# Performance work log

Hardware: AMD Instinct MI355X
Metric: run time of the kernel (lower is better)

## Reference

```python
import jax, jax.numpy as jnp
import numpy as np
from jax import lax

DN = ('NCHW', 'OIHW', 'NCHW')

def conv3x3(x, w, b):
    y = lax.conv_general_dilated(x, w, (1, 1), 'SAME', dimension_numbers=DN)
    return y + b[None, :, None, None]

def box_filter(x, ws):
    # depthwise WxW averaging conv, VALID after reflect pad
    C = x.shape[1]
    k = jnp.ones((C, 1, ws, ws), x.dtype) / (ws * ws)
    return lax.conv_general_dilated(x, k, (1, 1), 'VALID', feature_group_count=C,
                                    dimension_numbers=DN)

def compute_std_map(features, ws):
    N, C, H, W = features.shape
    pad = ws // 2
    fp = jnp.pad(features, ((0, 0), (0, 0), (pad, pad), (pad, pad)), mode='reflect')
    local_mean = box_filter(fp, ws)            # [N,C,H,W]
    local_mean_sq = box_filter(fp * fp, ws)
    local_var = jnp.clip(local_mean_sq - local_mean ** 2, 1e-6, None)
    if C == 4:
        cw = jax.nn.softmax(jnp.array([1.0, 1.5, 1.0, 1.5], features.dtype))
    else:
        cw = jax.nn.softmax(jnp.ones((C,), features.dtype))
    result = jnp.sum(jnp.sqrt(local_var) * cw[None, :, None, None], axis=1, keepdims=True)
    return result ** 0.8                        # [N,1,H,W]

def setup_inputs() -> dict:
    key = jax.random.key(0)
    ks = jax.random.split(key, 10)
    inp = {}
    inp['x'] = jax.random.normal(ks[0], (1, 4, 1024, 1024), jnp.float32)
    inp['w1'] = jax.random.normal(ks[1], (32, 4, 3, 3), jnp.float32) * (1.0 / np.sqrt(4 * 9))
    inp['b1'] = jax.random.normal(ks[2], (32,), jnp.float32) * 0.01
    inp['w2'] = jax.random.normal(ks[3], (16, 32, 3, 3), jnp.float32) * (1.0 / np.sqrt(32 * 9))
    inp['b2'] = jax.random.normal(ks[4], (16,), jnp.float32) * 0.01
    inp['w3'] = jax.random.normal(ks[5], (8, 16, 3, 3), jnp.float32) * (1.0 / np.sqrt(16 * 9))
    inp['b3'] = jax.random.normal(ks[6], (8,), jnp.float32) * 0.01
    inp['channel_weights'] = jnp.ones((4,), jnp.float32) / 4.0
    inp['fusion_w'] = jnp.full((1, 3, 1, 1), 1.0 / 3.0, jnp.float32) + \
        jax.random.normal(ks[7], (1, 3, 1, 1), jnp.float32) * 0.02
    inp['fusion_b'] = jnp.zeros((1,), jnp.float32)
    return inp

def reference(x, w1, b1, w2, b2, w3, b3, channel_weights, fusion_w, fusion_b):
    window_sizes = [11, 25, 49]
    # feature extractor
    f = jax.nn.leaky_relu(conv3x3(x, w1, b1), 0.2)
    f = jax.nn.leaky_relu(conv3x3(f, w2, b2), 0.2)
    f = conv3x3(f, w3, b3)                      # [B,8,H,W]
    # multi-scale std maps
    maps = jnp.concatenate([compute_std_map(f, ws) for ws in window_sizes], axis=1)  # [B,3,H,W]
    fused = jax.nn.relu(
        lax.conv_general_dilated(maps, fusion_w, (1, 1), 'VALID', dimension_numbers=DN)
        + fusion_b[None, :, None, None])        # [B,1,H,W]
    # adaptive thresholds
    std_flat = fused.reshape(-1)
    q25 = jnp.quantile(std_flat, 0.25)
    q75 = jnp.quantile(std_flat, 0.75)
    iqr75 = q75 - q25
    global_std = jnp.std(x, axis=(2, 3), keepdims=True, ddof=1)   # [B,4,1,1]
    lower = (q25 - 0.5 * iqr75) * jnp.ones_like(global_std)
    upper = (q75 + 0.5 * iqr75) * jnp.ones_like(global_std)
    gf = jnp.clip(global_std * 5.0, 0.5, 2.0)
    lower = lower * gf
    upper = upper * gf
    cwn = jax.nn.softmax(channel_weights).reshape(1, 4, 1, 1)
    channel_std = jnp.std(x * cwn, axis=(2, 3), keepdims=True, ddof=1)
    cf = jnp.clip(channel_std * 2.0, 0.8, 1.2)
    lower = lower * cf
    upper = upper * cf
    # texture mask
    q30 = jnp.quantile(std_flat, 0.3)
    q70 = jnp.quantile(std_flat, 0.7)
    lower_mean = jnp.mean(lower, axis=1, keepdims=True)           # [B,1,1,1]
    upper_mean = jnp.mean(upper, axis=1, keepdims=True)
    l_t = 0.5 * lower_mean + 0.5 * q30
    u_t = 0.5 * upper_mean + 0.5 * q70
    iqr = q70 - q30
    widen = iqr < 0.01
    l_t = jnp.where(widen, l_t - iqr, l_t)
    u_t = jnp.where(widen, u_t + iqr, u_t)
    diff = u_t - l_t
    mid0 = (l_t + u_t) / 2
    narrow = diff < 0.02
    l_t = jnp.where(narrow, mid0 - 0.01, l_t)
    u_t = jnp.where(narrow, mid0 + 0.01, u_t)
    midpoint = (l_t + u_t) / 2
    scale = u_t - l_t
    normalized = jax.nn.sigmoid(4.0 * (fused - midpoint) / scale)
    nm = jnp.mean(normalized)
    mask = jnp.where(nm > 0.65, 0.1 + 0.5 * normalized,
                     jnp.where(nm < 0.35, 0.2 + 0.5 * normalized,
                               0.15 + 0.55 * normalized))
    return mask
```

## Files before the change

### kernel.cpp

```cpp
#include <hip/hip_runtime.h>
#include <stdint.h>

constexpr int H = 1024, W = 1024;
constexpr int NPIX = H * W;
constexpr int PADM = 24;
constexpr int PROW = W + 2 * PADM;

constexpr size_t OFF_F1H   = 0;
constexpr size_t OFF_F1L   = 67108864;
constexpr size_t OFF_F2H   = 134217728;
constexpr size_t OFF_F2L   = 167772160;
constexpr size_t OFF_F3    = 0;
constexpr size_t OFF_HF    = 33554432;
constexpr size_t OFF_HF2   = 67108864;
constexpr size_t OFF_FUSED = 100663296;
constexpr size_t OFF_SMALL  = 201326592;
constexpr size_t OFF_PSTAT  = OFF_SMALL;
constexpr size_t OFF_NMSUM  = OFF_SMALL + 4096;
constexpr size_t OFF_HIST   = OFF_SMALL + 4160;
constexpr size_t OFF_RSTATE = OFF_HIST + 8192;
constexpr size_t OFF_SCAL   = OFF_RSTATE + 64;
constexpr size_t OFF_WT     = OFF_SCAL + 64;

using short8  = __attribute__((ext_vector_type(8))) short;
using short4v = __attribute__((ext_vector_type(4))) short;
using f32x4   = __attribute__((ext_vector_type(4))) float;

__device__ __forceinline__ int reflect1024(int j) {
    return j < 0 ? -j : (j > 1023 ? 2046 - j : j);
}
__device__ __forceinline__ unsigned short rne_bf16(float v) {
    uint32_t u = __float_as_uint(v);
    return (unsigned short)((u + 0x7FFFu + ((u >> 16) & 1u)) >> 16);
}
__device__ __forceinline__ float bf16f(unsigned short h) {
    return __uint_as_float(((uint32_t)h) << 16);
}

__device__ void wfrag_body(const float* __restrict__ w, unsigned short* __restrict__ wfH,
                           unsigned short* __restrict__ wfL, int CIN, int COUT, int NF, int S,
                           int blk) {
    int total = NF * S * 512;
    int e = blk * 256 + threadIdx.x;
    if (e >= total) return;
    int j = e & 7, l = (e >> 3) & 63;
    int rest = e >> 9;
    int s = rest % S, nf = rest / S;
    int k = s * 32 + ((l >> 4) << 3) + j;
    int n = (l & 15) + 16 * nf;
    float v = 0.f;
    if (k < 9 * CIN && n < COUT) {
        int kk = k / CIN, c = k % CIN;
        int ky = kk / 3, kx = kk - ky * 3;
        v = w[((n * CIN + c) * 3 + ky) * 3 + kx];
    }
    unsigned short h = rne_bf16(v);
    wfH[e] = h;
    wfL[e] = rne_bf16(v - bf16f(h));
}

__global__ void prep_kernel(const float* __restrict__ w1, const float* __restrict__ w2,
                            const float* __restrict__ w3,
                            unsigned short* wf1H, unsigned short* wf1L,
                            unsigned short* wf2H, unsigned short* wf2L,
                            unsigned short* wf3H, unsigned short* wf3L,
                            const float* __restrict__ x, double* __restrict__ pstats,
                            double* nmsum, uint32_t* hist, uint32_t* rstate) {
    __shared__ double sb1[256], sb2[256];
    const int b = blockIdx.x, tid = threadIdx.x;
    if (b == 0) {
        for (int i = tid; i < 2048; i += 256) hist[i] = 0u;
        if (tid == 0) nmsum[0] = 0.0;
        if (tid < 8) rstate[tid] = 0u;
        if (tid < 8) {
            const uint32_t ranks[8] = {262143u, 262144u, 314572u, 314573u,
                                       734002u, 734003u, 786431u, 786432u};
            rstate[8 + tid] = ranks[tid];
        }
    } else if (b < 9) {
        wfrag_body(w1, wf1H, wf1L, 4, 32, 2, 2, b - 1);
    } else if (b < 27) {
        wfrag_body(w2, wf2H, wf2L, 32, 16, 1, 9, b - 9);
    } else if (b < 37) {
        wfrag_body(w3, wf3H, wf3L, 16, 8, 1, 5, b - 27);
    } else {
        int sb = b - 37;
        int ch = sb >> 6, blk = sb & 63;
        const float* p = x + (size_t)ch * NPIX;
        double s1 = 0.0, s2 = 0.0;
        for (int i = blk * 256 + tid; i < NPIX; i += 64 * 256) {
            double v = (double)p[i];
            s1 += v; s2 += v * v;
        }
        sb1[tid] = s1; sb2[tid] = s2;
        __syncthreads();
        for (int off = 128; off > 0; off >>= 1) {
            if (tid < off) { sb1[tid] += sb1[tid + off]; sb2[tid] += sb2[tid + off]; }
            __syncthreads();
        }
        if (tid == 0) { pstats[sb * 2] = sb1[0]; pstats[sb * 2 + 1] = sb2[0]; }
    }
}

template <int CIN, int COUT, int S, bool LEAKY, int OUT_MODE, int IN_MODE, int MINW>
__global__ __launch_bounds__(256, MINW) void mconv_kernel(
        const void* __restrict__ inA, const void* __restrict__ inB,
        const unsigned short* __restrict__ wfH, const unsigned short* __restrict__ wfL,
        const float* __restrict__ bias, void* __restrict__ outA, void* __restrict__ outB) {
    constexpr int NF = (COUT + 15) / 16;
    constexpr int RS = 66 * CIN;
    __shared__ __align__(16) unsigned short Ah[6 * RS];
    __shared__ __align__(16) unsigned short Al[6 * RS];

    const int tid = threadIdx.x;
    const int bx = blockIdx.x * 64, by = blockIdx.y * 4;
    const int lane = tid & 63, rw = tid >> 6;

    if constexpr (IN_MODE == 1) {
        constexpr int CROW = RS / 8;
        constexpr int LCP  = (CIN == 32) ? 2 : 1;
        constexpr int TOT  = 12 * CROW;
        constexpr int NLOAD = (TOT + 255) / 256;
        const unsigned short* gh = (const unsigned short*)inA;
        const unsigned short* gl = (const unsigned short*)inB;

        short8 regs[NLOAD];
#pragma unroll
        for (int k = 0; k < NLOAD; ++k) {
            int idx = tid + k * 256;
            short8 v = short8{0, 0, 0, 0, 0, 0, 0, 0};
            if (idx < TOT) {
                int ar = idx / CROW;
                int j  = idx - ar * CROW;
                int r  = ar >> 1;
                int a  = ar & 1;
                int gy = by - 1 + r;
                int gx = bx - 1 + (j >> LCP);
                if ((unsigned)gy < 1024u && (unsigned)gx < 1024u) {
                    const unsigned short* g = (a ? gl : gh) +
                        ((size_t)gy << 10) * CIN + (size_t)(bx - 1) * CIN + (size_t)j * 8;
                    v = *(const short8*)g;
                }
            }
            regs[k] = v;
        }
#pragma unroll
        for (int k = 0; k < NLOAD; ++k) {
            int idx = tid + k * 256;
            if (idx < TOT) {
                int ar = idx / CROW;
                int j  = idx - ar * CROW;
                int r  = ar >> 1;
                int a  = ar & 1;
                unsigned short* dst = (a ? Al : Ah) + r * RS + j * 8;
                *(short8*)dst = regs[k];
            }
        }
    } else {
        constexpr int TOT = 6 * 4 * 66;
        constexpr int NLOAD = (TOT + 255) / 256;
        const float* xin = (const float*)inA;
        float regs[NLOAD];
#pragma unroll
        for (int k = 0; k < NLOAD; ++k) {
            int idx = tid + k * 256;
            float v = 0.f;
            if (idx < TOT) {
                int rc  = idx / 66;
                int px  = idx - rc * 66;
                int r   = rc >> 2, c = rc & 3;
                int gy = by - 1 + r, gx = bx - 1 + px;
                if ((unsigned)gy < 1024u && (unsigned)gx < 1024u)
                    v = xin[(size_t)c * NPIX + ((size_t)gy << 10) + gx];
            }
            regs[k] = v;
        }
#pragma unroll
        for (int k = 0; k < NLOAD; ++k) {
            int idx = tid + k * 256;
            if (idx < TOT) {
                int rc  = idx / 66;
                int px  = idx - rc * 66;
                int r   = rc >> 2, c = rc & 3;
                uint32_t u = __float_as_uint(regs[k]);
                Ah[r * RS + px * CIN + c] = (unsigned short)(u >> 16);
                Al[r * RS + px * CIN + c] =
                    rne_bf16(regs[k] - __uint_as_float(u & 0xFFFF0000u));
            }
        }
    }

    short8 wh[NF][S], wl[NF][S];
#pragma unroll
    for (int nf = 0; nf < NF; ++nf)
#pragma unroll
        for (int s = 0; s < S; ++s) {
            wh[nf][s] = *(const short8*)(wfH + (size_t)((nf * S + s) * 64 + lane) * 8);
            wl[nf][s] = *(const short8*)(wfL + (size_t)((nf * S + s) * 64 + lane) * 8);
        }

    const int nidx = lane & 15;
    f32x4 acc[4][NF];
#pragma unroll
    for (int nf = 0; nf < NF; ++nf) {
        float bv = (nidx + nf * 16 < COUT) ? bias[nidx + nf * 16] : 0.f;
#pragma unroll
        for (int t = 0; t < 4; ++t) acc[t][nf] = f32x4{bv, bv, bv, bv};
    }

    __syncthreads();

    if constexpr (CIN == 32) {
        const int base = rw * RS + (lane & 15) * 32 + (lane >> 4) * 8;
        const unsigned short* pah = Ah + base;
        const unsigned short* pal = Al + base;
#pragma unroll
        for (int s = 0; s < S; ++s) {
            const int ky = s / 3, kx = s - (s / 3) * 3;
#pragma unroll
            for (int t = 0; t < 4; ++t) {
                const int off = ky * RS + kx * 32 + t * 512;
                short8 a = *(const short8*)(pah + off);
                short8 b = *(const short8*)(pal + off);
#pragma unroll
                for (int nf = 0; nf < NF; ++nf) {
                    acc[t][nf] = __builtin_amdgcn_mfma_f32_16x16x32_bf16(a, wh[nf][s], acc[t][nf], 0, 0, 0);
                    acc[t][nf] = __builtin_amdgcn_mfma_f32_16x16x32_bf16(b, wh[nf][s], acc[t][nf], 0, 0, 0);
                    acc[t][nf] = __builtin_amdgcn_mfma_f32_16x16x32_bf16(a, wl[nf][s], acc[t][nf], 0, 0, 0);
                }
            }
        }
    } else if constexpr (CIN == 16) {
        const int g23 = lane >> 5;
        const int base = rw * RS + (lane & 15) * 16 + ((lane >> 4) & 1) * 8;
#pragma unroll
        for (int s = 0; s < S; ++s) {
            const int kk0 = 2 * s, kk1 = 2 * s + 1;
            const int O0 = (kk0 / 3) * RS + (kk0 - (kk0 / 3) * 3) * 16;
            const int O1 = (kk1 <= 8) ? (kk1 / 3) * RS + (kk1 - (kk1 / 3) * 3) * 16 : 0;
            const int offs = base + (g23 ? O1 : O0);
#pragma unroll
            for (int t = 0; t < 4; ++t) {
                short8 a = *(const short8*)(Ah + offs + t * 256);
                short8 b = *(const short8*)(Al + offs + t * 256);
#pragma unroll
                for (int nf = 0; nf < NF; ++nf) {
                    acc[t][nf] = __builtin_amdgcn_mfma_f32_16x16x32_bf16(a, wh[nf][s], acc[t][nf], 0, 0, 0);
                    acc[t][nf] = __builtin_amdgcn_mfma_f32_16x16x32_bf16(b, wh[nf][s], acc[t][nf], 0, 0, 0);
                    acc[t][nf] = __builtin_amdgcn_mfma_f32_16x16x32_bf16(a, wl[nf][s], acc[t][nf], 0, 0, 0);
                }
            }
        }
    } else {
        const int base = rw * RS + (lane & 15) * 4;
        const int g2 = (lane >> 4) * 2;
#pragma unroll
        for (int s = 0; s < S; ++s) {
            int kkA = s * 8 + g2, kkB = kkA + 1;
            int kyA = (kkA * 11) >> 5; int kxA = kkA - kyA * 3;
            int poA = (kkA <= 8) ? kyA * RS + kxA * 4 : 0;
            int kyB = (kkB * 11) >> 5; int kxB = kkB - kyB * 3;
            int poB = (kkB <= 8) ? kyB * RS + kxB * 4 : 0;
#pragma unroll
            for (int t = 0; t < 4; ++t) {
                union { short4v q[2]; short8 o; } ua, ub;
                ua.q[0] = *(const short4v*)(Ah + base + poA + t * 64);
                ua.q[1] = *(const short4v*)(Ah + base + poB + t * 64);
                ub.q[0] = *(const short4v*)(Al + base + poA + t * 64);
                ub.q[1] = *(const short4v*)(Al + base + poB + t * 64);
                short8 a = ua.o, b = ub.o;
#pragma unroll
                for (int nf = 0; nf < NF; ++nf) {
                    acc[t][nf] = __builtin_amdgcn_mfma_f32_16x16x32_bf16(a, wh[nf][s], acc[t][nf], 0, 0, 0);
                    acc[t][nf] = __builtin_amdgcn_mfma_f32_16x16x32_bf16(b, wh[nf][s], acc[t][nf], 0, 0, 0);
                    acc[t][nf] = __builtin_amdgcn_mfma_f32_16x16x32_bf16(a, wl[nf][s], acc[t][nf], 0, 0, 0);
                }
            }
        }
    }

    const int y = by + rw;
    const int mrow = (lane >> 4) * 4;
    if constexpr (OUT_MODE == 0) {
        __syncthreads();
        float* smem = (float*)Ah;
        if (nidx < COUT) {
#pragma unroll
            for (int t = 0; t < 4; ++t)
#pragma unroll
                for (int j = 0; j < 4; ++j) {
                    float v = acc[t][0][j];
                    if (LEAKY) v = v >= 0.f ? v : 0.2f * v;
                    smem[(nidx * 4 + rw) * 66 + t * 16 + mrow + j] = v;
                }
        }
        __syncthreads();
        float* outp = (float*)outA;
#pragma unroll
        for (int k = 0; k < COUT; ++k) {
            int i = tid + k * 256;
            int px = i & 63, r = (i >> 6) & 3, c = i >> 8;
            outp[(size_t)c * NPIX + ((size_t)(by + r) << 10) + bx + px] =
                smem[(c * 4 + r) * 66 + px];
        }
    } else {
        unsigned short* oh = (unsigned short*)outA;
        unsigned short* ol = (unsigned short*)outB;
#pragma unroll
        for (int t = 0; t < 4; ++t)
#pragma unroll
            for (int nf = 0; nf < NF; ++nf)
#pragma unroll
                for (int j = 0; j < 4; ++j) {
                    float v = acc[t][nf][j];
                    if (LEAKY) v = v >= 0.f ? v : 0.2f * v;
                    int x = bx + t * 16 + mrow + j;
                    size_t off = ((size_t)((y << 10) + x)) * COUT + nf * 16 + nidx;
                    uint32_t u = __float_as_uint(v);
                    oh[off] = (unsigned short)(u >> 16);
                    ol[off] = rne_bf16(v - __uint_as_float(u & 0xFFFF0000u));
                }
    }
}

__global__ void hbox_kernel(const float* __restrict__ f3, float* __restrict__ hf,
                            float* __restrict__ hf2, int p) {
    const int row = blockIdx.x, ch = blockIdx.y, tid = threadIdx.x;
    const float* src = f3 + ch * NPIX + row * W;
    __shared__ float sraw[PROW];
    __shared__ float Pf[PROW + 1], Pf2[PROW + 1];
    __shared__ float wtot[4], wtot2[4];

    for (int i = tid; i < PROW; i += 256)
        sraw[i] = src[reflect1024(i - PADM)];
    __syncthreads();

    float lf[5], lf2[5];
    float sf = 0.f, sf2 = 0.f;
    const int base = tid * 5;
#pragma unroll
    for (int j = 0; j < 5; ++j) {
        int idx = base + j;
        float v = (idx < PROW) ? sraw[idx] : 0.f;
        sf += v;      lf[j] = sf;
        sf2 += v * v; lf2[j] = sf2;
    }
    const int lane = tid & 63, wid = tid >> 6;
    float tf = sf, tf2 = sf2;
#pragma unroll
    for (int off = 1; off < 64; off <<= 1) {
        float a = __shfl_up(tf, off);
        float b = __shfl_up(tf2, off);
        if (lane >= off) { tf += a; tf2 += b; }
    }
    if (lane == 63) { wtot[wid] = tf; wtot2[wid] = tf2; }
    __syncthreads();
    float bse = 0.f, bse2 = 0.f;
    for (int w2 = 0; w2 < wid; ++w2) { bse += wtot[w2]; bse2 += wtot2[w2]; }
    float ex = bse + tf - sf, ex2 = bse2 + tf2 - sf2;
    if (base <= PROW) { Pf[base] = ex; Pf2[base] = ex2; }
#pragma unroll
    for (int j = 0; j < 5; ++j) {
        int idx = base + j + 1;
        if (idx <= PROW) { Pf[idx] = ex + lf[j]; Pf2[idx] = ex2 + lf2[j]; }
    }
    __syncthreads();

    float* df  = hf  + ch * NPIX + row * W;
    float* df2 = hf2 + ch * NPIX + row * W;
    for (int x = tid; x < W; x += 256) {
        int a = x + PADM - p, b = x + PADM + p + 1;
        df[x]  = Pf[b]  - Pf[a];
        df2[x] = Pf2[b] - Pf2[a];
    }
}

constexpr int VRS = 32;
__global__ __launch_bounds__(512) void vbox_kernel(const float* __restrict__ hf,
                                                   const float* __restrict__ hf2,
                                                   float* __restrict__ fused,
                                                   const float* __restrict__ fw,
                                                   const float* __restrict__ fb,
                                                   int kidx, int p, float inv_area) {
    const int tid = threadIdx.x;
    const int colIdx = tid & 63, ch = tid >> 6;
    const int col = blockIdx.x * 64 + colIdx;
    const int r0 = blockIdx.y * VRS;
    const float* pf  = hf  + ch * NPIX + col;
    const float* pf2 = hf2 + ch * NPIX + col;

    float S1 = 0.f, S2 = 0.f;
    for (int t = -p; t <= p; ++t) {
        int rr = reflect1024(r0 + t);
        S1 += pf[rr * W];
        S2 += pf2[rr * W];
    }

    const float w = fw[kidx];
    const float bias0 = fb[0];

    __shared__ float ssq[8][8][65];
    const int jj = tid >> 6, cc = tid & 63;
    for (int rb = r0; rb < r0 + VRS; rb += 8) {
#pragma unroll
        for (int j = 0; j < 8; ++j) {
            int r = rb + j;
            float m1 = S1 * inv_area, m2 = S2 * inv_area;
            float var = fmaxf(m2 - m1 * m1, 1e-6f);
            ssq[ch][j][colIdx] = sqrtf(var);
            int radd = reflect1024(r + 1 + p), rsub = reflect1024(r - p);
            S1 += pf[radd * W] - pf[rsub * W];
            S2 += pf2[radd * W] - pf2[rsub * W];
        }
        __syncthreads();
        float a = 0.f;
#pragma unroll
        for (int c8 = 0; c8 < 8; ++c8) a += ssq[c8][jj][cc];
        float m = powf(a * 0.125f, 0.8f);
        float* fp = fused + ((size_t)(rb + jj) << 10) + blockIdx.x * 64 + cc;
        if (kidx == 0)      *fp = bias0 + w * m;
        else if (kidx == 1) *fp = *fp + w * m;
        else                *fp = fmaxf(*fp + w * m, 0.f);
        __syncthreads();
    }
}

__global__ void radix_hist_kernel(const float* __restrict__ fused, uint32_t* __restrict__ hist,
                                  const uint32_t* __restrict__ rstate, int pass) {
    __shared__ uint32_t h[8][256];
    int tid = threadIdx.x;
    for (int i = tid; i < 2048; i += 256) ((uint32_t*)h)[i] = 0u;
    __syncthreads();

    uint32_t pref[8];
#pragma unroll
    for (int r = 0; r < 8; ++r) pref[r] = rstate[r];
    uint32_t maskHi = (pass == 0) ? 0u : (0xFFFFFFFFu << (32 - 8 * pass));
    int shift = 24 - 8 * pass;

    for (int i = blockIdx.x * blockDim.x + tid; i < NPIX; i += gridDim.x * blockDim.x) {
        uint32_t u = __float_as_uint(fused[i]);
        uint32_t key = (u & 0x80000000u) ? ~u : (u | 0x80000000u);
        uint32_t bin = (key >> shift) & 0xFFu;
        if (pass == 0) {
            atomicAdd(&h[0][bin], 1u);
        } else {
#pragma unroll
            for (int r = 0; r < 8; ++r) {
                if (((key ^ pref[r]) & maskHi) == 0u)
                    atomicAdd(&h[r][bin], 1u);
            }
        }
    }
    __syncthreads();
    if (pass == 0) {
        for (int i = tid; i < 256; i += 256) {
            uint32_t v = h[0][i];
            if (v)
                for (int r = 0; r < 8; ++r) atomicAdd(&hist[r * 256 + i], v);
        }
    } else {
        for (int i = tid; i < 2048; i += 256) {
            uint32_t v = ((uint32_t*)h)[i];
            if (v) atomicAdd(&hist[i], v);
        }
    }
}

__device__ __forceinline__ float key_to_float(uint32_t k) {
    uint32_t u = (k & 0x80000000u) ? (k & 0x7FFFFFFFu) : ~k;
    return __uint_as_float(u);
}

__global__ void radix_scan_kernel(uint32_t* __restrict__ hist, uint32_t* __restrict__ rstate,
                                  int pass, const double* __restrict__ pstats,
                                  const float* __restrict__ cw, float* __restrict__ scal) {
    int tid = threadIdx.x;
    int shift = 24 - 8 * pass;
    const int lane = tid & 63, wv = tid >> 6;
    __shared__ uint32_t wsum[4];
    __shared__ uint32_t fkey[8];
    for (int r = 0; r < 8; ++r) {
        uint32_t c = hist[r * 256 + tid];
        uint32_t sc = c;
#pragma unroll
        for (int off = 1; off < 64; off <<= 1) {
            uint32_t t = __shfl_up(sc, off);
            if (lane >= off) sc += t;
        }
        if (lane == 63) wsum[wv] = sc;
        __syncthreads();
        uint32_t base = 0;
        for (int w2 = 0; w2 < wv; ++w2) base += wsum[w2];
        uint32_t incl = base + sc, excl = incl - c;
        uint32_t lr = rstate[8 + r];
        if (lr >= excl && lr < incl) {
            uint32_t nk = rstate[r] | (((uint32_t)tid) << shift);
            rstate[r] = nk;
            rstate[8 + r] = lr - excl;
            if (pass == 3) fkey[r] = nk;
        }
        hist[r * 256 + tid] = 0u;
        __syncthreads();
    }

    if (pass == 3) {
        double s1 = pstats[2 * tid], s2 = pstats[2 * tid + 1];
#pragma unroll
        for (int off = 32; off > 0; off >>= 1) {
            s1 += __shfl_down(s1, off);
            s2 += __shfl_down(s2, off);
        }
        __shared__ double gs[4][2];
        if ((tid & 63) == 0) { gs[tid >> 6][0] = s1; gs[tid >> 6][1] = s2; }
        __syncthreads();
        if (tid == 0) {
            float v[8];
#pragma unroll
            for (int r = 0; r < 8; ++r) v[r] = key_to_float(fkey[r]);
            float q25 = v[0] + 0.75f * (v[1] - v[0]);
            float q30 = v[2] + 0.5f * (v[3] - v[2]);
            float q70 = v[4] + 0.5f * (v[5] - v[4]);
            float q75 = v[6] + 0.25f * (v[7] - v[6]);

            const double N = (double)NPIX;
            float gstd[4];
#pragma unroll
            for (int c = 0; c < 4; ++c) {
                double a1 = gs[c][0], a2 = gs[c][1];
                double var = (a2 - a1 * a1 / N) / (N - 1.0);
                gstd[c] = (float)sqrt(var > 0.0 ? var : 0.0);
            }
            float m = fmaxf(fmaxf(cw[0], cw[1]), fmaxf(cw[2], cw[3]));
            float e0 = expf(cw[0] - m), e1 = expf(cw[1] - m);
            float e2 = expf(cw[2] - m), e3 = expf(cw[3] - m);
            float se = e0 + e1 + e2 + e3;
            float cwn[4] = {e0 / se, e1 / se, e2 / se, e3 / se};

            float iqr75 = q75 - q25;
            float low0 = q25 - 0.5f * iqr75;
            float up0  = q75 + 0.5f * iqr75;
            float lsum = 0.f, usum = 0.f;
#pragma unroll
            for (int c = 0; c < 4; ++c) {
                float gf = fminf(fmaxf(gstd[c] * 5.f, 0.5f), 2.f);
                float cs = cwn[c] * gstd[c];
                float cf = fminf(fmaxf(cs * 2.f, 0.8f), 1.2f);
                lsum += low0 * gf * cf;
                usum += up0 * gf * cf;
            }
            float lmean = 0.25f * lsum, umean = 0.25f * usum;
            float l_t = 0.5f * lmean + 0.5f * q30;
            float u_t = 0.5f * umean + 0.5f * q70;
            float iqr = q70 - q30;
            if (iqr < 0.01f) { l_t -= iqr; u_t += iqr; }
            float diff = u_t - l_t;
            float mid0 = 0.5f * (l_t + u_t);
            if (diff < 0.02f) { l_t = mid0 - 0.01f; u_t = mid0 + 0.01f; }
            scal[0] = 0.5f * (l_t + u_t);
            scal[1] = u_t - l_t;
        }
    }
}

__global__ void sigmoid_kernel(const float* __restrict__ fused, const float* __restrict__ scal,
                               double* __restrict__ nmsum) {
    float mid = scal[0], sc = scal[1];
    float inv = 4.0f / sc;
    float local = 0.f;
    for (int i = blockIdx.x * blockDim.x + threadIdx.x; i < NPIX; i += gridDim.x * blockDim.x) {
        float t = (fused[i] - mid) * inv;
        local += 1.0f / (1.0f + expf(-t));
    }
    __shared__ float red[256];
    red[threadIdx.x] = local;
    __syncthreads();
    for (int off = 128; off > 0; off >>= 1) {
        if (threadIdx.x < off) red[threadIdx.x] += red[threadIdx.x + off];
        __syncthreads();
    }
    if (threadIdx.x == 0) atomicAdd(nmsum, (double)red[0]);
}

__global__ void final_kernel(const float* __restrict__ fused, const float* __restrict__ scal,
                             const double* __restrict__ nmsum, float* __restrict__ out) {
    float nm = (float)(nmsum[0] / (double)NPIX);
    float a, b;
    if (nm > 0.65f)      { a = 0.10f; b = 0.50f; }
    else if (nm < 0.35f) { a = 0.20f; b = 0.50f; }
    else                 { a = 0.15f; b = 0.55f; }
    float mid = scal[0], inv = 4.0f / scal[1];
    for (int i = blockIdx.x * blockDim.x + threadIdx.x; i < NPIX; i += gridDim.x * blockDim.x) {
        float t = (fused[i] - mid) * inv;
        float n = 1.0f / (1.0f + expf(-t));
        out[i] = a + b * n;
    }
}

extern "C" void kernel_launch(void* const* d_in, const int* in_sizes, int n_in,
                              void* d_out, int out_size, void* d_ws, size_t ws_size,
                              hipStream_t stream) {
    const float* x   = (const float*)d_in[0];
    const float* w1  = (const float*)d_in[1];
    const float* b1  = (const float*)d_in[2];
    const float* w2  = (const float*)d_in[3];
    const float* b2  = (const float*)d_in[4];
    const float* w3  = (const float*)d_in[5];
    const float* b3  = (const float*)d_in[6];
    const float* cw  = (const float*)d_in[7];
    const float* fw  = (const float*)d_in[8];
    const float* fb  = (const float*)d_in[9];

    char* ws = (char*)d_ws;
    unsigned short* f1h = (unsigned short*)(ws + OFF_F1H);
    unsigned short* f1l = (unsigned short*)(ws + OFF_F1L);
    unsigned short* f2h = (unsigned short*)(ws + OFF_F2H);
    unsigned short* f2l = (unsigned short*)(ws + OFF_F2L);
    float* f3    = (float*)(ws + OFF_F3);
    float* hf    = (float*)(ws + OFF_HF);
    float* hf2   = (float*)(ws + OFF_HF2);
    float* fused = (float*)(ws + OFF_FUSED);
    double* pstats = (double*)(ws + OFF_PSTAT);
    double* nmsum  = (double*)(ws + OFF_NMSUM);
    uint32_t* hist   = (uint32_t*)(ws + OFF_HIST);
    uint32_t* rstate = (uint32_t*)(ws + OFF_RSTATE);
    float* scal = (float*)(ws + OFF_SCAL);
    unsigned short* wf1H = (unsigned short*)(ws + OFF_WT);
    unsigned short* wf1L = wf1H + 2048;
    unsigned short* wf2H = wf1L + 2048;
    unsigned short* wf2L = wf2H + 4608;
    unsigned short* wf3H = wf2L + 4608;
    unsigned short* wf3L = wf3H + 2560;

    prep_kernel<<<293, 256, 0, stream>>>(w1, w2, w3, wf1H, wf1L, wf2H, wf2L, wf3H, wf3L,
                                         x, pstats, nmsum, hist, rstate);

    dim3 cgrid(16, 256);
    mconv_kernel<4, 32, 2, true, 1, 0, 4><<<cgrid, 256, 0, stream>>>(
        x, nullptr, wf1H, wf1L, b1, f1h, f1l);
    mconv_kernel<32, 16, 9, true, 1, 1, 3><<<cgrid, 256, 0, stream>>>(
        f1h, f1l, wf2H, wf2L, b2, f2h, f2l);
    mconv_kernel<16, 8, 5, false, 0, 1, 4><<<cgrid, 256, 0, stream>>>(
        f2h, f2l, wf3H, wf3L, b3, f3, nullptr);

    const int wss[3] = {11, 25, 49};
    for (int k = 0; k < 3; ++k) {
        int p = wss[k] / 2;
        float inv_area = 1.0f / (float)(wss[k] * wss[k]);
        hbox_kernel<<<dim3(H, 8), 256, 0, stream>>>(f3, hf, hf2, p);
        vbox_kernel<<<dim3(W / 64, H / VRS), 512, 0, stream>>>(hf, hf2, fused, fw, fb,
                                                               k, p, inv_area);
    }

    for (int pass = 0; pass < 4; ++pass) {
        radix_hist_kernel<<<512, 256, 0, stream>>>(fused, hist, rstate, pass);
        radix_scan_kernel<<<1, 256, 0, stream>>>(hist, rstate, pass, pstats, cw, scal);
    }

    sigmoid_kernel<<<1024, 256, 0, stream>>>(fused, scal, nmsum);
    final_kernel<<<1024, 256, 0, stream>>>(fused, scal, nmsum, (float*)d_out);
}
```

Baseline: 359.3 us.

## Interleave bf16 hi/lo feature planes and stage conv outputs through LDS

```diff
diff --git a/kernel.cpp b/kernel.cpp
--- a/kernel.cpp
+++ b/kernel.cpp
@@ -6,10 +6,8 @@
 constexpr int PADM = 24;
 constexpr int PROW = W + 2 * PADM;
 
-constexpr size_t OFF_F1H   = 0;
-constexpr size_t OFF_F1L   = 67108864;
-constexpr size_t OFF_F2H   = 134217728;
-constexpr size_t OFF_F2L   = 167772160;
+constexpr size_t OFF_F1P   = 0;
+constexpr size_t OFF_F2P   = 134217728;
 constexpr size_t OFF_F3    = 0;
 constexpr size_t OFF_HF    = 33554432;
 constexpr size_t OFF_HF2   = 67108864;
@@ -25,6 +23,8 @@
 using short8  = __attribute__((ext_vector_type(8))) short;
 using short4v = __attribute__((ext_vector_type(4))) short;
 using f32x4   = __attribute__((ext_vector_type(4))) float;
+using uint2v  = __attribute__((ext_vector_type(2))) unsigned int;
+using uint4v  = __attribute__((ext_vector_type(4))) unsigned int;
 
 __device__ __forceinline__ int reflect1024(int j) {
     return j < 0 ? -j : (j > 1023 ? 2046 - j : j);
@@ -35,6 +35,12 @@
 }
 __device__ __forceinline__ float bf16f(unsigned short h) {
     return __uint_as_float(((uint32_t)h) << 16);
+}
+__device__ __forceinline__ uint32_t pack_hl(float v) {
+    uint32_t u = __float_as_uint(v);
+    unsigned short hh = (unsigned short)(u >> 16);
+    unsigned short ll = rne_bf16(v - __uint_as_float(u & 0xFFFF0000u));
+    return (uint32_t)hh | ((uint32_t)ll << 16);
 }
 
 __device__ void wfrag_body(const float* __restrict__ w, unsigned short* __restrict__ wfH,
@@ -104,43 +110,43 @@
 
 template <int CIN, int COUT, int S, bool LEAKY, int OUT_MODE, int IN_MODE, int MINW>
 __global__ __launch_bounds__(256, MINW) void mconv_kernel(
-        const void* __restrict__ inA, const void* __restrict__ inB,
+        const void* __restrict__ in,
         const unsigned short* __restrict__ wfH, const unsigned short* __restrict__ wfL,
-        const float* __restrict__ bias, void* __restrict__ outA, void* __restrict__ outB) {
+        const float* __restrict__ bias, void* __restrict__ out) {
     constexpr int NF = (COUT + 15) / 16;
     constexpr int RS = 66 * CIN;
-    __shared__ __align__(16) unsigned short Ah[6 * RS];
-    __shared__ __align__(16) unsigned short Al[6 * RS];
+    constexpr int PSTR = COUT + 4;
+    constexpr int STAGEB = 2 * (6 * RS) * 2;
+    constexpr int EPIB = (OUT_MODE == 1) ? (4 * 64 * PSTR * 4) : (COUT * 4 * 66 * 4);
+    constexpr int LBYTES = STAGEB > EPIB ? STAGEB : EPIB;
+    __shared__ __align__(16) unsigned char LB[LBYTES];
+    unsigned short* Ah = (unsigned short*)LB;
+    unsigned short* Al = Ah + 6 * RS;
 
     const int tid = threadIdx.x;
     const int bx = blockIdx.x * 64, by = blockIdx.y * 4;
     const int lane = tid & 63, rw = tid >> 6;
 
     if constexpr (IN_MODE == 1) {
-        constexpr int CROW = RS / 8;
-        constexpr int LCP  = (CIN == 32) ? 2 : 1;
-        constexpr int TOT  = 12 * CROW;
+        constexpr int CPP = CIN / 4;
+        constexpr int CROW = 66 * CPP;
+        constexpr int TOT = 6 * CROW;
         constexpr int NLOAD = (TOT + 255) / 256;
-        const unsigned short* gh = (const unsigned short*)inA;
-        const unsigned short* gl = (const unsigned short*)inB;
-
-        short8 regs[NLOAD];
+        const uint32_t* gp = (const uint32_t*)in;
+
+        uint4v regs[NLOAD];
 #pragma unroll
         for (int k = 0; k < NLOAD; ++k) {
             int idx = tid + k * 256;
-            short8 v = short8{0, 0, 0, 0, 0, 0, 0, 0};
+            uint4v v = uint4v{0u, 0u, 0u, 0u};
             if (idx < TOT) {
-                int ar = idx / CROW;
-                int j  = idx - ar * CROW;
-                int r  = ar >> 1;
-                int a  = ar & 1;
+                int r = idx / CROW;
+                int j = idx - r * CROW;
                 int gy = by - 1 + r;
-                int gx = bx - 1 + (j >> LCP);
-                if ((unsigned)gy < 1024u && (unsigned)gx < 1024u) {
-                    const unsigned short* g = (a ? gl : gh) +
-                        ((size_t)gy << 10) * CIN + (size_t)(bx - 1) * CIN + (size_t)j * 8;
-                    v = *(const short8*)g;
-                }
+                int gx = bx - 1 + j / CPP;
+                if ((unsigned)gy < 1024u && (unsigned)gx < 1024u)
+                    v = *(const uint4v*)(gp + ((size_t)gy << 10) * CIN +
+                                         (size_t)(bx - 1) * CIN + (size_t)j * 4);
             }
             regs[k] = v;
         }
@@ -148,18 +154,24 @@
         for (int k = 0; k < NLOAD; ++k) {
             int idx = tid + k * 256;
             if (idx < TOT) {
-                int ar = idx / CROW;
-                int j  = idx - ar * CROW;
-                int r  = ar >> 1;
-                int a  = ar & 1;
-                unsigned short* dst = (a ? Al : Ah) + r * RS + j * 8;
-                *(short8*)dst = regs[k];
+                int r = idx / CROW;
+                int j = idx - r * CROW;
+                int px = j / CPP, c0 = (j - px * CPP) * 4;
+                uint32_t p0 = regs[k].x, p1 = regs[k].y, p2 = regs[k].z, p3 = regs[k].w;
+                uint2v hh, ll;
+                hh.x = __builtin_amdgcn_perm(p1, p0, 0x05040100u);
+                hh.y = __builtin_amdgcn_perm(p3, p2, 0x05040100u);
+                ll.x = __builtin_amdgcn_perm(p1, p0, 0x07060302u);
+                ll.y = __builtin_amdgcn_perm(p3, p2, 0x07060302u);
+                int off = r * RS + px * CIN + c0;
+                *(uint2v*)(Ah + off) = hh;
+                *(uint2v*)(Al + off) = ll;
             }
         }
     } else {
         constexpr int TOT = 6 * 4 * 66;
         constexpr int NLOAD = (TOT + 255) / 256;
-        const float* xin = (const float*)inA;
+        const float* xin = (const float*)in;
         float regs[NLOAD];
 #pragma unroll
         for (int k = 0; k < NLOAD; ++k) {
@@ -279,11 +291,10 @@
         }
     }
 
-    const int y = by + rw;
     const int mrow = (lane >> 4) * 4;
     if constexpr (OUT_MODE == 0) {
         __syncthreads();
-        float* smem = (float*)Ah;
+        float* smem = (float*)LB;
         if (nidx < COUT) {
 #pragma unroll
             for (int t = 0; t < 4; ++t)
@@ -295,7 +306,7 @@
                 }
         }
         __syncthreads();
-        float* outp = (float*)outA;
+        float* outp = (float*)out;
 #pragma unroll
         for (int k = 0; k < COUT; ++k) {
             int i = tid + k * 256;
@@ -304,8 +315,8 @@
                 smem[(c * 4 + r) * 66 + px];
         }
     } else {
-        unsigned short* oh = (unsigned short*)outA;
-        unsigned short* ol = (unsigned short*)outB;
+        __syncthreads();
+        uint32_t* pk = (uint32_t*)LB;
 #pragma unroll
         for (int t = 0; t < 4; ++t)
 #pragma unroll
@@ -314,12 +325,25 @@
                 for (int j = 0; j < 4; ++j) {
                     float v = acc[t][nf][j];
                     if (LEAKY) v = v >= 0.f ? v : 0.2f * v;
-                    int x = bx + t * 16 + mrow + j;
-                    size_t off = ((size_t)((y << 10) + x)) * COUT + nf * 16 + nidx;
-                    uint32_t u = __float_as_uint(v);
-                    oh[off] = (unsigned short)(u >> 16);
-                    ol[off] = rne_bf16(v - __uint_as_float(u & 0xFFFF0000u));
+                    int xl = t * 16 + mrow + j;
+                    pk[(rw * 64 + xl) * PSTR + nf * 16 + nidx] = pack_hl(v);
                 }
+        __syncthreads();
+        uint32_t* gp = (uint32_t*)out;
+        constexpr int ROWU = 64 * COUT;
+        constexpr int NU4 = 4 * ROWU / 4;
+#pragma unroll
+        for (int k = 0; k < (NU4 + 255) / 256; ++k) {
+            int i = tid + k * 256;
+            if (i < NU4) {
+                int e = i * 4;
+                int r = e / ROWU;
+                int rem = e - r * ROWU;
+                int px = rem / COUT, c = rem - px * COUT;
+                uint4v val = *(const uint4v*)&pk[(r * 64 + px) * PSTR + c];
+                *(uint4v*)(gp + ((size_t)(((by + r) << 10) + bx + px)) * COUT + c) = val;
+            }
+        }
     }
 }
 
@@ -612,10 +636,8 @@
     const float* fb  = (const float*)d_in[9];
 
     char* ws = (char*)d_ws;
-    unsigned short* f1h = (unsigned short*)(ws + OFF_F1H);
-    unsigned short* f1l = (unsigned short*)(ws + OFF_F1L);
-    unsigned short* f2h = (unsigned short*)(ws + OFF_F2H);
-    unsigned short* f2l = (unsigned short*)(ws + OFF_F2L);
+    uint32_t* f1p = (uint32_t*)(ws + OFF_F1P);
+    uint32_t* f2p = (uint32_t*)(ws + OFF_F2P);
     float* f3    = (float*)(ws + OFF_F3);
     float* hf    = (float*)(ws + OFF_HF);
     float* hf2   = (float*)(ws + OFF_HF2);
@@ -637,11 +659,11 @@
 
     dim3 cgrid(16, 256);
     mconv_kernel<4, 32, 2, true, 1, 0, 4><<<cgrid, 256, 0, stream>>>(
-        x, nullptr, wf1H, wf1L, b1, f1h, f1l);
+        x, wf1H, wf1L, b1, f1p);
     mconv_kernel<32, 16, 9, true, 1, 1, 3><<<cgrid, 256, 0, stream>>>(
-        f1h, f1l, wf2H, wf2L, b2, f2h, f2l);
+        f1p, wf2H, wf2L, b2, f2p);
     mconv_kernel<16, 8, 5, false, 0, 1, 4><<<cgrid, 256, 0, stream>>>(
-        f2h, f2l, wf3H, wf3L, b3, f3, nullptr);
+        f2p, wf3H, wf3L, b3, f3);
 
     const int wss[3] = {11, 25, 49};
     for (int k = 0; k < 3; ++k) {
```

New measurement: 359.6 us. No clear change (+0.1%).
